# Kernel tuning notes

Measured on AMD Instinct MI355X. Metric: run time of the kernel, lower is better.

Reference implementation:

```python
import jax, jax.numpy as jnp
import numpy as np

BS, SEQ, IN_DIM, EMB = 64, 1024, 512, 1024
HID = EMB // 2  # MLP hidden = embed_dim//2 = 512
RATIO = 0.3
K = max(1, int((SEQ - 2) * RATIO))  # 306
MASK_VALUE = -10000.0
BN_EPS = 1e-5


def setup_inputs() -> dict:
    key = jax.random.key(0)
    ks = jax.random.split(key, 12)
    features = jax.random.normal(ks[0], (BS, SEQ, IN_DIM), dtype=jnp.float32)
    atten = jax.random.normal(ks[1], (BS, SEQ, SEQ), dtype=jnp.float32)
    # variable-length token ids, pad_id = 0
    lengths = jax.random.randint(ks[2], (BS,), K + 14, SEQ + 1)
    tokens = jax.random.randint(ks[3], (BS, SEQ), 1, 30000)
    text = jnp.where(jnp.arange(SEQ)[None, :] < lengths[:, None], tokens, 0).astype(jnp.int64)
    s = 0.02
    lin_w = jax.random.normal(ks[4], (IN_DIM, EMB), dtype=jnp.float32) * s
    lin_b = jnp.zeros((EMB,), dtype=jnp.float32)
    w1 = jax.random.normal(ks[5], (IN_DIM, HID), dtype=jnp.float32) * s
    b1 = jnp.zeros((HID,), dtype=jnp.float32)
    g1 = jnp.ones((HID,), dtype=jnp.float32)
    be1 = jnp.zeros((HID,), dtype=jnp.float32)
    w2 = jax.random.normal(ks[6], (HID, EMB), dtype=jnp.float32) * s
    b2 = jnp.zeros((EMB,), dtype=jnp.float32)
    return {"features": features, "atten": atten, "text": text,
            "lin_w": lin_w, "lin_b": lin_b, "w1": w1, "b1": b1,
            "g1": g1, "be1": be1, "w2": w2, "b2": b2}


def _forward(features, atten, text, lin_w, lin_b, w1, b1, g1, be1, w2, b2):
    bs, seq_len, _ = atten.shape
    atten = jnp.nan_to_num(atten, nan=0.0, posinf=0.0, neginf=0.0)
    mask = (text != 0).astype(jnp.float32)                       # (bs, seq)
    token_lens = jnp.maximum(jnp.sum(text != 0, axis=1), 1)       # (bs,)
    eos_pos = jnp.clip(token_lens - 1, 0, seq_len - 1)            # (bs,)
    # mask column 0 and column eos_pos (per batch) across all rows
    col = jnp.arange(seq_len)[None, :]
    col_mask = (col == 0) | (col == eos_pos[:, None])             # (bs, seq)
    atten = jnp.where(col_mask[:, None, :], MASK_VALUE, atten)
    # masked_fill where token is pad (columns)
    atten = jnp.where(mask[:, None, :] == 0, MASK_VALUE, atten)
    atten = jax.nn.softmax(atten, axis=1)                         # softmax over rows (dim=1)
    # select the eos row per batch, weight by mask
    atten_sel = jnp.take_along_axis(atten, eos_pos[:, None, None], axis=1)[:, 0, :] * mask
    _, topk_idx = jax.lax.top_k(atten_sel, K)                     # (bs, K)
    feats_k = jnp.take_along_axis(features, topk_idx[:, :, None], axis=1)  # (bs, K, D)
    norm = jnp.maximum(jnp.linalg.norm(feats_k, axis=-1, keepdims=True), 1e-6)
    feats_k = feats_k / norm
    cap_emb = feats_k @ lin_w + lin_b                             # (bs, K, EMB)
    # MLP: Linear -> BatchNorm1d(train-mode batch stats) -> ReLU -> Linear
    xf = feats_k.reshape(bs * K, -1)
    h = xf @ w1 + b1                                              # (bs*K, HID)
    mu = jnp.mean(h, axis=0)
    var = jnp.mean((h - mu) ** 2, axis=0)                         # biased var
    h = (h - mu) / jnp.sqrt(var + BN_EPS) * g1 + be1
    h = jax.nn.relu(h)
    feats_mlp = (h @ w2 + b2).reshape(bs, K, -1)
    fused = cap_emb + feats_mlp                                   # (bs, K, EMB)
    # variable-length top-1 pooling: max over first pool_lens[b] tokens
    pool_lens = jnp.clip(token_lens - 2, 1, K)
    valid = jnp.arange(K)[None, :] < pool_lens[:, None]           # (bs, K)
    out = jnp.max(jnp.where(valid[:, :, None], fused, -jnp.inf), axis=1)
    return out.astype(jnp.float32)


def reference(features, atten, text, lin_w, lin_b, w1, b1, g1, be1, w2, b2):
    return _forward(features, atten, text, lin_w, lin_b, w1, b1, g1, be1, w2, b2)
```

## Files before the change

kernel.cpp:

```cpp
#include <hip/hip_runtime.h>
#include <cstdint>
#include <cstddef>

#define BS 64
#define SEQ 1024
#define IN_DIM 512
#define EMB 1024
#define HID 512
#define KSEL 306
#define MROWS (BS * KSEL)

typedef __bf16 bf16_t;
typedef bf16_t bf16x8 __attribute__((ext_vector_type(8)));
typedef bf16_t bf16x4 __attribute__((ext_vector_type(4)));
typedef float f32x4 __attribute__((ext_vector_type(4)));

__device__ __forceinline__ void async16(const void* g, void* l) {
  __builtin_amdgcn_global_load_lds(
      (const __attribute__((address_space(1))) unsigned int*)g,
      (__attribute__((address_space(3))) unsigned int*)l, 16, 0, 0);
}

__global__ void k_meta(const int* __restrict__ text, int* __restrict__ eos) {
  int b = blockIdx.x;
  __shared__ int cnt;
  if (threadIdx.x == 0) cnt = 0;
  __syncthreads();
  int local = 0;
  for (int i = threadIdx.x; i < SEQ; i += blockDim.x)
    local += (text[b * SEQ + i] != 0) ? 1 : 0;
  atomicAdd(&cnt, local);
  __syncthreads();
  if (threadIdx.x == 0) {
    int L = cnt > 1 ? cnt : 1;
    int e = L - 1;
    if (e > SEQ - 1) e = SEQ - 1;
    eos[b] = e;
  }
}

__global__ void k_colsum(const float* __restrict__ atten, float* __restrict__ colsum) {
  int b = blockIdx.x;
  int r0 = blockIdx.y << 7;
  int c = (blockIdx.z << 8) | threadIdx.x;
  const float* base = atten + ((size_t)b << 20) + ((size_t)r0 << 10) + c;
  float s = 0.f;
#pragma unroll 4
  for (int r = 0; r < 128; ++r) {
    float x = base[(size_t)r << 10];
    if (!isfinite(x)) x = 0.f;
    s += __expf(x - 12.f);
  }
  atomicAdd(&colsum[(b << 10) | c], s);
}

__global__ void k_selval(const float* __restrict__ atten, const int* __restrict__ text,
                         const int* __restrict__ eos, const float* __restrict__ colsum,
                         float* __restrict__ selval) {
  int b = blockIdx.x >> 2;
  int c = ((blockIdx.x & 3) << 8) | threadIdx.x;
  int e = eos[b];
  float v = atten[((size_t)b << 20) + ((size_t)e << 10) + c];
  if (!isfinite(v)) v = 0.f;
  int tok = text[(b << 10) | c];
  float res;
  if (tok == 0) res = 0.f;
  else if (c == 0 || c == e) res = 1.f / 1024.f;
  else res = __expf(v - 12.f) / colsum[(b << 10) | c];
  selval[(b << 10) | c] = res;
}

__global__ void k_topk(const float* __restrict__ selval, int* __restrict__ selidx) {
  int b = blockIdx.x;
  __shared__ float vals[SEQ];
  int i = threadIdx.x;
  vals[i] = selval[(b << 10) + i];
  __syncthreads();
  float vc = vals[i];
  int rank = 0;
  for (int j = 0; j < SEQ; ++j) {
    float vj = vals[j];
    rank += (vj > vc || (vj == vc && j < i)) ? 1 : 0;
  }
  if (rank < KSEL) selidx[b * KSEL + rank] = i;
}

__global__ void k_gather(const float* __restrict__ features, const int* __restrict__ sel,
                         bf16_t* __restrict__ xcat) {
  int row = blockIdx.x;
  int b = row / KSEL;
  int k = row - b * KSEL;
  int idx = sel[b * KSEL + k];
  const float4* src = (const float4*)(features + (((size_t)b << 10) + idx) * IN_DIM);
  float4 v = src[threadIdx.x];
  float ss = v.x * v.x + v.y * v.y + v.z * v.z + v.w * v.w;
#pragma unroll
  for (int off = 32; off > 0; off >>= 1) ss += __shfl_down(ss, off, 64);
  __shared__ float wsum[2];
  int lane = threadIdx.x & 63, wid = threadIdx.x >> 6;
  if (lane == 0) wsum[wid] = ss;
  __syncthreads();
  float total = wsum[0] + wsum[1];
  float scale = 1.f / fmaxf(sqrtf(total), 1e-6f);
  bf16x4 o;
  o[0] = (bf16_t)(v.x * scale);
  o[1] = (bf16_t)(v.y * scale);
  o[2] = (bf16_t)(v.z * scale);
  o[3] = (bf16_t)(v.w * scale);
  *(bf16x4*)(xcat + (size_t)row * EMB + (threadIdx.x << 2)) = o;
}

__global__ void k_transpose_bf16(const float* __restrict__ src, int srcld,
                                 bf16_t* __restrict__ dst, int dstld) {
  __shared__ float tile[32][33];
  int k0 = blockIdx.x << 5, n0 = blockIdx.y << 5;
  int tx = threadIdx.x, ty = threadIdx.y;
#pragma unroll
  for (int i = 0; i < 4; i++)
    tile[ty + 8 * i][tx] = src[(size_t)(k0 + ty + 8 * i) * srcld + n0 + tx];
  __syncthreads();
#pragma unroll
  for (int i = 0; i < 4; i++)
    dst[(size_t)(n0 + ty + 8 * i) * dstld + k0 + tx] = (bf16_t)tile[tx][ty + 8 * i];
}

__global__ void k_biasc(const float* __restrict__ lin_b, const float* __restrict__ b2,
                        float* __restrict__ biasC) {
  int n = threadIdx.x;
  biasC[n] = lin_b[n] + b2[n];
}

__global__ __launch_bounds__(256, 2) void k_mfma_gemm(
    const bf16_t* __restrict__ A, int lda, const bf16_t* __restrict__ Bt, int ldb,
    const float* __restrict__ bias, float* __restrict__ C, int ldc, int K) {
  __shared__ __align__(16) bf16_t As[128 * 32];
  __shared__ __align__(16) bf16_t Bs[128 * 32];
  int tid = threadIdx.x;
  int m0 = blockIdx.x << 7, n0 = blockIdx.y << 7;
  int wave = tid >> 6, lane = tid & 63;
  int wm = (wave >> 1) << 6, wn = (wave & 1) << 6;
  int lrow = lane & 15, quad = lane >> 4;

  f32x4 acc[4][4];
#pragma unroll
  for (int i = 0; i < 4; i++)
#pragma unroll
    for (int j = 0; j < 4; j++) acc[i][j] = (f32x4){0.f, 0.f, 0.f, 0.f};

  int c0 = tid, c1 = 256 + tid;
  int ar0 = c0 >> 2, ak0 = (c0 & 3) << 3;
  int ar1 = c1 >> 2, ak1 = (c1 & 3) << 3;
  const bf16_t* Ap0 = A + (size_t)(m0 + ar0) * lda + ak0;
  const bf16_t* Ap1 = A + (size_t)(m0 + ar1) * lda + ak1;
  const bf16_t* Bp0 = Bt + (size_t)(n0 + ar0) * ldb + ak0;
  const bf16_t* Bp1 = Bt + (size_t)(n0 + ar1) * ldb + ak1;

  for (int k0 = 0; k0 < K; k0 += 32) {
    async16(Ap0 + k0, &As[c0 << 3]);
    async16(Ap1 + k0, &As[c1 << 3]);
    async16(Bp0 + k0, &Bs[c0 << 3]);
    async16(Bp1 + k0, &Bs[c1 << 3]);
    __syncthreads();

    bf16x8 af[4], bfr[4];
#pragma unroll
    for (int i = 0; i < 4; i++)
      af[i] = *(const bf16x8*)&As[((wm + (i << 4) + lrow) << 5) + (quad << 3)];
#pragma unroll
    for (int j = 0; j < 4; j++)
      bfr[j] = *(const bf16x8*)&Bs[((wn + (j << 4) + lrow) << 5) + (quad << 3)];
#pragma unroll
    for (int i = 0; i < 4; i++)
#pragma unroll
      for (int j = 0; j < 4; j++)
        acc[i][j] = __builtin_amdgcn_mfma_f32_16x16x32_bf16(af[i], bfr[j], acc[i][j], 0, 0, 0);
    __syncthreads();
  }

#pragma unroll
  for (int j = 0; j < 4; j++) {
    int n = n0 + wn + (j << 4) + lrow;
    float bv = bias ? bias[n] : 0.f;
#pragma unroll
    for (int i = 0; i < 4; i++) {
      int mbase = m0 + wm + (i << 4) + (quad << 2);
#pragma unroll
      for (int r = 0; r < 4; r++)
        C[(size_t)(mbase + r) * ldc + n] = acc[i][j][r] + bv;
    }
  }
}

__global__ void k_bnstats(const float* __restrict__ h, float* __restrict__ stats) {
  int r0 = blockIdx.x << 7;
  int c = threadIdx.x;
  float s0 = 0, q0 = 0, s1 = 0, q1 = 0;
  for (int r = 0; r < 128; ++r) {
    const float* row = h + (size_t)(r0 + r) * HID;
    float x0 = row[c], x1 = row[c + 256];
    s0 += x0; q0 += x0 * x0;
    s1 += x1; q1 += x1 * x1;
  }
  atomicAdd(&stats[c], s0);
  atomicAdd(&stats[HID + c], q0);
  atomicAdd(&stats[c + 256], s1);
  atomicAdd(&stats[HID + c + 256], q1);
}

__global__ void k_bnparam(const float* __restrict__ stats, const float* __restrict__ g,
                          const float* __restrict__ be, float* __restrict__ scsh) {
  int c = threadIdx.x;
  float inv = 1.f / (float)MROWS;
  float mu = stats[c] * inv;
  float var = stats[HID + c] * inv - mu * mu;
  var = fmaxf(var, 0.f);
  float sc = g[c] * rsqrtf(var + 1e-5f);
  scsh[c] = sc;
  scsh[HID + c] = fmaf(-mu, sc, be[c]);
}

__global__ void k_bnapply(const float* __restrict__ h, const float* __restrict__ scsh,
                          bf16_t* __restrict__ xcat) {
  size_t idx = (size_t)blockIdx.x * blockDim.x + threadIdx.x;
  float4 x = ((const float4*)h)[idx];
  int c = (int)(idx & 127) << 2;
  size_t row = idx >> 7;
  float a0 = fmaxf(fmaf(x.x, scsh[c + 0], scsh[HID + c + 0]), 0.f);
  float a1 = fmaxf(fmaf(x.y, scsh[c + 1], scsh[HID + c + 1]), 0.f);
  float a2 = fmaxf(fmaf(x.z, scsh[c + 2], scsh[HID + c + 2]), 0.f);
  float a3 = fmaxf(fmaf(x.w, scsh[c + 3], scsh[HID + c + 3]), 0.f);
  bf16x4 o;
  o[0] = (bf16_t)a0; o[1] = (bf16_t)a1; o[2] = (bf16_t)a2; o[3] = (bf16_t)a3;
  *(bf16x4*)(xcat + row * EMB + 512 + c) = o;
}

__global__ void k_maxpool(const float* __restrict__ fused, float* __restrict__ out) {
  int b = blockIdx.x;
  int c = (blockIdx.y << 8) | threadIdx.x;
  const float* p = fused + (((size_t)b * KSEL) << 10) + c;
  float m = -3.4e38f;
  for (int k = 0; k < KSEL; ++k) m = fmaxf(m, p[(size_t)k << 10]);
  out[(b << 10) | c] = m;
}

extern "C" void kernel_launch(void* const* d_in, const int* in_sizes, int n_in,
                              void* d_out, int out_size, void* d_ws, size_t ws_size,
                              hipStream_t stream) {
  const float* features = (const float*)d_in[0];
  const float* atten    = (const float*)d_in[1];
  const int*   text     = (const int*)d_in[2];
  const float* lin_w    = (const float*)d_in[3];
  const float* lin_b    = (const float*)d_in[4];
  const float* w1       = (const float*)d_in[5];
  const float* b1       = (const float*)d_in[6];
  const float* g1       = (const float*)d_in[7];
  const float* be1      = (const float*)d_in[8];
  const float* w2       = (const float*)d_in[9];
  const float* b2       = (const float*)d_in[10];
  float* out = (float*)d_out;

  char* ws = (char*)d_ws;
  int*    eos    = (int*)(ws + 0);
  float*  stats  = (float*)(ws + 256);
  float*  scsh   = (float*)(ws + 4608);
  float*  biasC  = (float*)(ws + 8704);
  float*  colsum = (float*)(ws + 12800);
  float*  selval = (float*)(ws + 274944);
  int*    selidx = (int*)(ws + 537088);
  bf16_t* w1t    = (bf16_t*)(ws + 615424);
  bf16_t* wcatt  = (bf16_t*)(ws + 1139712);
  bf16_t* xcat   = (bf16_t*)(ws + 3236864);
  float*  h      = (float*)(ws + 43344896UL);
  float*  fused  = (float*)(ws + 83452928UL);

  hipMemsetAsync(stats, 0, 4096, stream);
  hipMemsetAsync(colsum, 0, 64 * 1024 * sizeof(float), stream);

  k_meta<<<BS, 256, 0, stream>>>(text, eos);
  k_colsum<<<dim3(BS, 8, 4), 256, 0, stream>>>(atten, colsum);
  k_selval<<<BS * 4, 256, 0, stream>>>(atten, text, eos, colsum, selval);
  k_topk<<<BS, 1024, 0, stream>>>(selval, selidx);
  k_gather<<<MROWS, 128, 0, stream>>>(features, selidx, xcat);

  k_transpose_bf16<<<dim3(16, 16), dim3(32, 8), 0, stream>>>(w1, HID, w1t, IN_DIM);
  k_transpose_bf16<<<dim3(16, 32), dim3(32, 8), 0, stream>>>(lin_w, EMB, wcatt, EMB);
  k_transpose_bf16<<<dim3(16, 32), dim3(32, 8), 0, stream>>>(w2, EMB, wcatt + 512, EMB);
  k_biasc<<<1, EMB, 0, stream>>>(lin_b, b2, biasC);

  k_mfma_gemm<<<dim3(MROWS / 128, HID / 128), 256, 0, stream>>>(
      xcat, EMB, w1t, IN_DIM, b1, h, HID, IN_DIM);

  k_bnstats<<<MROWS / 128, 256, 0, stream>>>(h, stats);
  k_bnparam<<<1, HID, 0, stream>>>(stats, g1, be1, scsh);
  k_bnapply<<<(MROWS * (HID / 4)) / 256, 256, 0, stream>>>(h, scsh, xcat);

  k_mfma_gemm<<<dim3(MROWS / 128, EMB / 128), 256, 0, stream>>>(
      xcat, EMB, wcatt, EMB, biasC, fused, EMB, EMB);

  k_maxpool<<<dim3(BS, 4), 256, 0, stream>>>(fused, out);
}
```

Baseline: 676.8 us.

## Fuse maxpool and BN statistics into GEMM epilogues; drop colsum atomics

```diff
diff --git a/kernel.cpp b/kernel.cpp
--- a/kernel.cpp
+++ b/kernel.cpp
@@ -1,6 +1,7 @@
 #include <hip/hip_runtime.h>
 #include <cstdint>
 #include <cstddef>
+#include <cmath>
 
 #define BS 64
 #define SEQ 1024
@@ -21,7 +22,15 @@
       (__attribute__((address_space(3))) unsigned int*)l, 16, 0, 0);
 }
 
-__global__ void k_meta(const int* __restrict__ text, int* __restrict__ eos) {
+__device__ __forceinline__ void atomicMaxF(float* a, float v) {
+  if (v >= 0.f)
+    atomicMax((int*)a, __float_as_int(v));
+  else
+    atomicMin((unsigned int*)a, __float_as_uint(v));
+}
+
+__global__ void k_meta(const int* __restrict__ text, int* __restrict__ eos,
+                       float* __restrict__ out) {
   int b = blockIdx.x;
   __shared__ int cnt;
   if (threadIdx.x == 0) cnt = 0;
@@ -30,6 +39,8 @@
   for (int i = threadIdx.x; i < SEQ; i += blockDim.x)
     local += (text[b * SEQ + i] != 0) ? 1 : 0;
   atomicAdd(&cnt, local);
+  for (int c = threadIdx.x; c < EMB; c += blockDim.x)
+    out[(b << 10) + c] = -INFINITY;
   __syncthreads();
   if (threadIdx.x == 0) {
     int L = cnt > 1 ? cnt : 1;
@@ -39,34 +50,39 @@
   }
 }
 
-__global__ void k_colsum(const float* __restrict__ atten, float* __restrict__ colsum) {
+__global__ void k_colsum(const float* __restrict__ atten, float* __restrict__ part) {
   int b = blockIdx.x;
-  int r0 = blockIdx.y << 7;
-  int c = (blockIdx.z << 8) | threadIdx.x;
+  int r0 = blockIdx.y << 6;
+  int c = threadIdx.x << 2;
   const float* base = atten + ((size_t)b << 20) + ((size_t)r0 << 10) + c;
-  float s = 0.f;
+  float4 s = {0.f, 0.f, 0.f, 0.f};
 #pragma unroll 4
-  for (int r = 0; r < 128; ++r) {
-    float x = base[(size_t)r << 10];
-    if (!isfinite(x)) x = 0.f;
-    s += __expf(x - 12.f);
-  }
-  atomicAdd(&colsum[(b << 10) | c], s);
+  for (int r = 0; r < 64; ++r) {
+    float4 x = *(const float4*)(base + ((size_t)r << 10));
+    s.x += __expf((isfinite(x.x) ? x.x : 0.f) - 12.f);
+    s.y += __expf((isfinite(x.y) ? x.y : 0.f) - 12.f);
+    s.z += __expf((isfinite(x.z) ? x.z : 0.f) - 12.f);
+    s.w += __expf((isfinite(x.w) ? x.w : 0.f) - 12.f);
+  }
+  *(float4*)&part[((((size_t)blockIdx.y << 6) | b) << 10) | c] = s;
 }
 
 __global__ void k_selval(const float* __restrict__ atten, const int* __restrict__ text,
-                         const int* __restrict__ eos, const float* __restrict__ colsum,
+                         const int* __restrict__ eos, const float* __restrict__ part,
                          float* __restrict__ selval) {
   int b = blockIdx.x >> 2;
   int c = ((blockIdx.x & 3) << 8) | threadIdx.x;
   int e = eos[b];
+  float cs = 0.f;
+#pragma unroll
+  for (int p = 0; p < 16; ++p) cs += part[(((p << 6) | b) << 10) | c];
   float v = atten[((size_t)b << 20) + ((size_t)e << 10) + c];
   if (!isfinite(v)) v = 0.f;
   int tok = text[(b << 10) | c];
   float res;
   if (tok == 0) res = 0.f;
   else if (c == 0 || c == e) res = 1.f / 1024.f;
-  else res = __expf(v - 12.f) / colsum[(b << 10) | c];
+  else res = __expf(v - 12.f) / cs;
   selval[(b << 10) | c] = res;
 }
 
@@ -130,9 +146,11 @@
   biasC[n] = lin_b[n] + b2[n];
 }
 
+template <int MODE>
 __global__ __launch_bounds__(256, 2) void k_mfma_gemm(
     const bf16_t* __restrict__ A, int lda, const bf16_t* __restrict__ Bt, int ldb,
-    const float* __restrict__ bias, float* __restrict__ C, int ldc, int K) {
+    const float* __restrict__ bias, float* __restrict__ C, int ldc, int K,
+    float* __restrict__ stats, float* __restrict__ outmax) {
   __shared__ __align__(16) bf16_t As[128 * 32];
   __shared__ __align__(16) bf16_t Bs[128 * 32];
   int tid = threadIdx.x;
@@ -177,34 +195,61 @@
     __syncthreads();
   }
 
-#pragma unroll
-  for (int j = 0; j < 4; j++) {
-    int n = n0 + wn + (j << 4) + lrow;
-    float bv = bias ? bias[n] : 0.f;
-#pragma unroll
-    for (int i = 0; i < 4; i++) {
-      int mbase = m0 + wm + (i << 4) + (quad << 2);
-#pragma unroll
-      for (int r = 0; r < 4; r++)
-        C[(size_t)(mbase + r) * ldc + n] = acc[i][j][r] + bv;
+  if (MODE == 0) {
+#pragma unroll
+    for (int j = 0; j < 4; j++) {
+      int n = n0 + wn + (j << 4) + lrow;
+      float bv = bias[n];
+      float s = 0.f, q = 0.f;
+#pragma unroll
+      for (int i = 0; i < 4; i++) {
+        int mbase = m0 + wm + (i << 4) + (quad << 2);
+#pragma unroll
+        for (int r = 0; r < 4; r++) {
+          float v = acc[i][j][r] + bv;
+          C[(size_t)(mbase + r) * ldc + n] = v;
+          s += v;
+          q += v * v;
+        }
+      }
+      s += __shfl_xor(s, 16, 64);
+      s += __shfl_xor(s, 32, 64);
+      q += __shfl_xor(q, 16, 64);
+      q += __shfl_xor(q, 32, 64);
+      if (quad == 0) {
+        atomicAdd(&stats[n], s);
+        atomicAdd(&stats[HID + n], q);
+      }
     }
-  }
-}
-
-__global__ void k_bnstats(const float* __restrict__ h, float* __restrict__ stats) {
-  int r0 = blockIdx.x << 7;
-  int c = threadIdx.x;
-  float s0 = 0, q0 = 0, s1 = 0, q1 = 0;
-  for (int r = 0; r < 128; ++r) {
-    const float* row = h + (size_t)(r0 + r) * HID;
-    float x0 = row[c], x1 = row[c + 256];
-    s0 += x0; q0 += x0 * x0;
-    s1 += x1; q1 += x1 * x1;
-  }
-  atomicAdd(&stats[c], s0);
-  atomicAdd(&stats[HID + c], q0);
-  atomicAdd(&stats[c + 256], s1);
-  atomicAdd(&stats[HID + c + 256], q1);
+  } else {
+    int mw = m0 + wm;
+    int b0w = mw / KSEL;
+    int cut = (b0w + 1) * KSEL;
+#pragma unroll
+    for (int j = 0; j < 4; j++) {
+      int n = n0 + wn + (j << 4) + lrow;
+      float bv = bias[n];
+      float mx0 = -INFINITY, mx1 = -INFINITY;
+#pragma unroll
+      for (int i = 0; i < 4; i++) {
+#pragma unroll
+        for (int r = 0; r < 4; r++) {
+          int m = mw + (i << 4) + (quad << 2) + r;
+          float v = acc[i][j][r] + bv;
+          if (m < cut) mx0 = fmaxf(mx0, v);
+          else mx1 = fmaxf(mx1, v);
+        }
+      }
+      mx0 = fmaxf(mx0, __shfl_xor(mx0, 16, 64));
+      mx0 = fmaxf(mx0, __shfl_xor(mx0, 32, 64));
+      mx1 = fmaxf(mx1, __shfl_xor(mx1, 16, 64));
+      mx1 = fmaxf(mx1, __shfl_xor(mx1, 32, 64));
+      if (quad == 0) {
+        atomicMaxF(&outmax[(b0w << 10) + n], mx0);
+        if (cut < mw + 64) atomicMaxF(&outmax[((b0w + 1) << 10) + n], mx1);
+      }
+    }
+  }
 }
 
 __global__ void k_bnparam(const float* __restrict__ stats, const float* __restrict__ g,
@@ -232,15 +277,6 @@
   bf16x4 o;
   o[0] = (bf16_t)a0; o[1] = (bf16_t)a1; o[2] = (bf16_t)a2; o[3] = (bf16_t)a3;
   *(bf16x4*)(xcat + row * EMB + 512 + c) = o;
-}
-
-__global__ void k_maxpool(const float* __restrict__ fused, float* __restrict__ out) {
-  int b = blockIdx.x;
-  int c = (blockIdx.y << 8) | threadIdx.x;
-  const float* p = fused + (((size_t)b * KSEL) << 10) + c;
-  float m = -3.4e38f;
-  for (int k = 0; k < KSEL; ++k) m = fmaxf(m, p[(size_t)k << 10]);
-  out[(b << 10) | c] = m;
 }
 
 extern "C" void kernel_launch(void* const* d_in, const int* in_sizes, int n_in,
@@ -264,21 +300,19 @@
   float*  stats  = (float*)(ws + 256);
   float*  scsh   = (float*)(ws + 4608);
   float*  biasC  = (float*)(ws + 8704);
-  float*  colsum = (float*)(ws + 12800);
-  float*  selval = (float*)(ws + 274944);
-  int*    selidx = (int*)(ws + 537088);
-  bf16_t* w1t    = (bf16_t*)(ws + 615424);
-  bf16_t* wcatt  = (bf16_t*)(ws + 1139712);
-  bf16_t* xcat   = (bf16_t*)(ws + 3236864);
-  float*  h      = (float*)(ws + 43344896UL);
-  float*  fused  = (float*)(ws + 83452928UL);
+  float*  part   = (float*)(ws + 12800);
+  float*  selval = (float*)(ws + 4207104UL);
+  int*    selidx = (int*)(ws + 4469248UL);
+  bf16_t* w1t    = (bf16_t*)(ws + 4547584UL);
+  bf16_t* wcatt  = (bf16_t*)(ws + 5071872UL);
+  bf16_t* xcat   = (bf16_t*)(ws + 7169024UL);
+  float*  h      = (float*)(ws + 47277056UL);
 
   hipMemsetAsync(stats, 0, 4096, stream);
-  hipMemsetAsync(colsum, 0, 64 * 1024 * sizeof(float), stream);
-
-  k_meta<<<BS, 256, 0, stream>>>(text, eos);
-  k_colsum<<<dim3(BS, 8, 4), 256, 0, stream>>>(atten, colsum);
-  k_selval<<<BS * 4, 256, 0, stream>>>(atten, text, eos, colsum, selval);
+
+  k_meta<<<BS, 256, 0, stream>>>(text, eos, out);
+  k_colsum<<<dim3(BS, 16), 256, 0, stream>>>(atten, part);
+  k_selval<<<BS * 4, 256, 0, stream>>>(atten, text, eos, part, selval);
   k_topk<<<BS, 1024, 0, stream>>>(selval, selidx);
   k_gather<<<MROWS, 128, 0, stream>>>(features, selidx, xcat);
 
@@ -287,15 +321,12 @@
   k_transpose_bf16<<<dim3(16, 32), dim3(32, 8), 0, stream>>>(w2, EMB, wcatt + 512, EMB);
   k_biasc<<<1, EMB, 0, stream>>>(lin_b, b2, biasC);
 
-  k_mfma_gemm<<<dim3(MROWS / 128, HID / 128), 256, 0, stream>>>(
-      xcat, EMB, w1t, IN_DIM, b1, h, HID, IN_DIM);
-
-  k_bnstats<<<MROWS / 128, 256, 0, stream>>>(h, stats);
+  k_mfma_gemm<0><<<dim3(MROWS / 128, HID / 128), 256, 0, stream>>>(
+      xcat, EMB, w1t, IN_DIM, b1, h, HID, IN_DIM, stats, nullptr);
+
   k_bnparam<<<1, HID, 0, stream>>>(stats, g1, be1, scsh);
   k_bnapply<<<(MROWS * (HID / 4)) / 256, 256, 0, stream>>>(h, scsh, xcat);
 
-  k_mfma_gemm<<<dim3(MROWS / 128, EMB / 128), 256, 0, stream>>>(
-      xcat, EMB, wcatt, EMB, biasC, fused, EMB, EMB);
-
-  k_maxpool<<<dim3(BS, 4), 256, 0, stream>>>(fused, out);
-}
+  k_mfma_gemm<1><<<dim3(MROWS / 128, EMB / 128), 256, 0, stream>>>(
+      xcat, EMB, wcatt, EMB, biasC, nullptr, 0, EMB, nullptr, out);
+}
```

After: 612.5 us. 9.5% less time.
